# Kernel optimization log

Measured on AMD Instinct MI355X. Metric: run time of the kernel, lower is better.

The kernel has to match this reference:

```python
import jax, jax.numpy as jnp
import numpy as np

SEQ, HID, IN, THETA = 4096, 512, 512, 5


def setup_inputs() -> dict:
    key = jax.random.key(0)
    k0, k1, k2, k3, k4 = jax.random.split(key, 5)
    return {
        "input": jax.random.normal(k0, (1, SEQ, IN), jnp.float32),
        "internal": jax.random.normal(k1, (THETA + 1, SEQ, HID), jnp.float32) * 0.1,
        "state": jnp.zeros((1, 1, HID), jnp.float32),
        "W_ih": jax.random.normal(k2, (HID, IN), jnp.float32) / np.sqrt(IN).astype(np.float32),
        "W_hh": jax.random.normal(k3, (HID, HID), jnp.float32) / np.sqrt(HID).astype(np.float32),
        "b": jax.random.normal(k4, (HID,), jnp.float32) * 0.01,
        "theta": THETA,
    }


def reference(input, internal, state, W_ih, W_hh, b, theta):
    # Unbatched path (batched=False), continuousTheta=False, trunc >= seq (no detach).
    # Cell: h' = tanh(x @ W_ih.T + h @ W_hh.T + b + noise); out = h'.
    x = input[0]                      # [S, I]
    pre_x = x @ W_ih.T + b            # [S, H] precompute input drive
    h0 = state[0, 0]                  # [H]

    # Main recurrence over the sequence (theta index 0 of internal drives it).
    def step(h, px_n):
        px, n = px_n
        h_new = jnp.tanh(px + h @ W_hh.T + n)
        return h_new, h_new

    _, hs = jax.lax.scan(step, h0, (pre_x, internal[0]))   # hs: [S, H]

    # Theta rollouts: padded input is zero, so drive = b + noise. The rollout at
    # every timestep starts from that timestep's main state -> vectorize over S
    # and scan over the theta axis.
    def roll(H, n):
        H_new = jnp.tanh(b + H @ W_hh.T + n)
        return H_new, H_new

    _, Hs = jax.lax.scan(roll, hs, internal[1:])           # Hs: [theta, S, H]

    outputs = jnp.concatenate([hs[None], Hs], axis=0)      # [theta+1, S, H]
    final_state = hs[-1][None, None]                        # [1, 1, H]
    return outputs, final_state
```

## Files before the change

kernel.cpp:

```cpp
#include <hip/hip_runtime.h>
#include <cstdint>
#include <cstddef>

#define SEQ 4096
#define HID 512
#define NTHETA 5
#define NBLK 4
#define RPB 128
#define SENT_BITS 0x40000000u

typedef unsigned long long u64;

__device__ __forceinline__ float tanh_fast(float x) {
  x = fminf(fmaxf(x, -20.0f), 20.0f);
  const float e = __expf(2.0f * x);
  return (e - 1.0f) / (e + 1.0f);
}

__device__ __forceinline__ uint4 load_x4_sc1(const unsigned* p) {
  uint4 u;
  asm volatile("global_load_dwordx4 %0, %1, off sc1\n\ts_waitcnt vmcnt(0)"
               : "=v"(u) : "v"(p) : "memory");
  return u;
}

__device__ __forceinline__ float red16(float v) {
  int p;
  p = __builtin_amdgcn_update_dpp(0, __float_as_int(v), 0xB1, 0xF, 0xF, true);
  v += __int_as_float(p);
  p = __builtin_amdgcn_update_dpp(0, __float_as_int(v), 0x4E, 0xF, 0xF, true);
  v += __int_as_float(p);
  v += __int_as_float(__builtin_amdgcn_ds_swizzle(__float_as_int(v), 0x101F));
  p = __builtin_amdgcn_update_dpp(0, __float_as_int(v), 0x128, 0xF, 0xF, true);
  v += __int_as_float(p);
  return v;
}

__device__ __forceinline__ int swz(int f) {
  return (f & ~7) | ((f ^ (f >> 3)) & 7);
}

__global__ __launch_bounds__(256) void gemm_bias_noise(
    const float* __restrict__ A, const float* __restrict__ W,
    const float* __restrict__ bias, const float* __restrict__ noise,
    float* __restrict__ C, int K, int doTanh)
{
  const int N = HID;
  const int bm = blockIdx.y, bn = blockIdx.x;
  const int tid = threadIdx.x;
  const int tx = tid & 15, ty = tid >> 4;
  const int row0 = bm * 64, col0 = bn * 64;
  __shared__ float As[16][68];
  __shared__ float Ws[16][68];
  float acc[4][4] = {{0.f, 0.f, 0.f, 0.f}, {0.f, 0.f, 0.f, 0.f},
                     {0.f, 0.f, 0.f, 0.f}, {0.f, 0.f, 0.f, 0.f}};
  const int lrow = tid >> 2, lkq = tid & 3;
  for (int kt = 0; kt < K; kt += 16) {
    const float4 av = *(const float4*)&A[(size_t)(row0 + lrow) * K + kt + lkq * 4];
    const float4 wv = *(const float4*)&W[(size_t)(col0 + lrow) * K + kt + lkq * 4];
    __syncthreads();
    As[lkq * 4 + 0][lrow] = av.x; As[lkq * 4 + 1][lrow] = av.y;
    As[lkq * 4 + 2][lrow] = av.z; As[lkq * 4 + 3][lrow] = av.w;
    Ws[lkq * 4 + 0][lrow] = wv.x; Ws[lkq * 4 + 1][lrow] = wv.y;
    Ws[lkq * 4 + 2][lrow] = wv.z; Ws[lkq * 4 + 3][lrow] = wv.w;
    __syncthreads();
#pragma unroll
    for (int k = 0; k < 16; ++k) {
      const float4 a = *(const float4*)&As[k][ty * 4];
      const float4 bq = *(const float4*)&Ws[k][tx * 4];
      const float a4[4] = {a.x, a.y, a.z, a.w};
      const float b4[4] = {bq.x, bq.y, bq.z, bq.w};
#pragma unroll
      for (int i = 0; i < 4; ++i)
#pragma unroll
        for (int j = 0; j < 4; ++j)
          acc[i][j] = fmaf(a4[i], b4[j], acc[i][j]);
    }
  }
  const float4 bv = *(const float4*)&bias[col0 + tx * 4];
#pragma unroll
  for (int i = 0; i < 4; ++i) {
    const int row = row0 + ty * 4 + i;
    const float4 nv = *(const float4*)&noise[(size_t)row * N + col0 + tx * 4];
    float4 o;
    o.x = acc[i][0] + bv.x + nv.x;
    o.y = acc[i][1] + bv.y + nv.y;
    o.z = acc[i][2] + bv.z + nv.z;
    o.w = acc[i][3] + bv.w + nv.w;
    if (doTanh) {
      o.x = tanh_fast(o.x); o.y = tanh_fast(o.y);
      o.z = tanh_fast(o.z); o.w = tanh_fast(o.w);
    }
    *(float4*)&C[(size_t)row * N + col0 + tx * 4] = o;
  }
}

__global__ void fill_sentinel(uint4* __restrict__ p, int n4) {
  const int i = blockIdx.x * blockDim.x + threadIdx.x;
  if (i < n4) p[i] = make_uint4(SENT_BITS, SENT_BITS, SENT_BITS, SENT_BITS);
}

__global__ __launch_bounds__(1024, 4) void recurrence(
    const float* __restrict__ Whh, const float* __restrict__ drive,
    const float* __restrict__ h0, unsigned* __restrict__ hexch)
{
  const int blk = blockIdx.x;
  const int base = blk * RPB;
  const int tid = threadIdx.x;
  const int i = tid >> 4;
  const int j = tid & 15;
  const int r0 = base + 2 * i;

  __shared__ __align__(16) float hbuf[2][HID];

  float4 w0[8], w1[8];
#pragma unroll
  for (int c = 0; c < 8; ++c) {
    w0[c] = *(const float4*)&Whh[(size_t)r0 * HID + 32 * j + 4 * c];
    w1[c] = *(const float4*)&Whh[(size_t)(r0 + 1) * HID + 32 * j + 4 * c];
  }

  const int ch = (tid < blk * 32) ? tid : tid + 32;
  const int wslot = swz(ch);
  const int z0 = swz(r0 >> 2) * 4 + (r0 & 3);

  if (tid < HID) hbuf[0][swz(tid >> 2) * 4 + (tid & 3)] = h0[tid];

  for (int t = 0; t < SEQ; ++t) {
    const int buf = t & 1;

    float2 dr = make_float2(0.f, 0.f);
    if (j == 0) dr = *(const float2*)&drive[(size_t)t * HID + r0];

    if (t > 0 && tid < 96) {
      const unsigned* src = &hexch[(size_t)(t - 1) * HID + 4 * ch];
      uint4 u = load_x4_sc1(src);
      int it = 0;
      while (u.x == SENT_BITS || u.y == SENT_BITS ||
             u.z == SENT_BITS || u.w == SENT_BITS) {
        if ((++it & 7) == 0) {
          u.x = __hip_atomic_load(src + 0, __ATOMIC_RELAXED,
                                  __HIP_MEMORY_SCOPE_AGENT);
          u.y = __hip_atomic_load(src + 1, __ATOMIC_RELAXED,
                                  __HIP_MEMORY_SCOPE_AGENT);
          u.z = __hip_atomic_load(src + 2, __ATOMIC_RELAXED,
                                  __HIP_MEMORY_SCOPE_AGENT);
          u.w = __hip_atomic_load(src + 3, __ATOMIC_RELAXED,
                                  __HIP_MEMORY_SCOPE_AGENT);
        } else {
          u = load_x4_sc1(src);
        }
      }
      ((uint4*)hbuf[buf])[wslot] = u;
    }
    __syncthreads();
    asm volatile("" :: "v"(dr.x), "v"(dr.y));

    float a00 = 0.f, a01 = 0.f, a02 = 0.f, a03 = 0.f;
    float a10 = 0.f, a11 = 0.f, a12 = 0.f, a13 = 0.f;
#pragma unroll
    for (int c = 0; c < 8; ++c) {
      const float4 h4 = *(const float4*)&hbuf[buf][(8 * j + ((c ^ j) & 7)) * 4];
      a00 = fmaf(w0[c].x, h4.x, a00);
      a01 = fmaf(w0[c].y, h4.y, a01);
      a02 = fmaf(w0[c].z, h4.z, a02);
      a03 = fmaf(w0[c].w, h4.w, a03);
      a10 = fmaf(w1[c].x, h4.x, a10);
      a11 = fmaf(w1[c].y, h4.y, a11);
      a12 = fmaf(w1[c].z, h4.z, a12);
      a13 = fmaf(w1[c].w, h4.w, a13);
    }
    float s0 = red16((a00 + a01) + (a02 + a03));
    float s1 = red16((a10 + a11) + (a12 + a13));

    if (j == 0) {
      const float y0 = tanh_fast(s0 + dr.x);
      const float y1 = tanh_fast(s1 + dr.y);
      const u64 pk = (u64)__float_as_uint(y0) | ((u64)__float_as_uint(y1) << 32);
      __hip_atomic_store((u64*)&hexch[(size_t)t * HID + r0], pk,
                         __ATOMIC_RELAXED, __HIP_MEMORY_SCOPE_AGENT);
      *(float2*)&hbuf[buf ^ 1][z0] = make_float2(y0, y1);
    }
  }
}

__global__ void copy_final(const float* __restrict__ src, float* __restrict__ dst) {
  dst[threadIdx.x] = src[threadIdx.x];
}

extern "C" void kernel_launch(void* const* d_in, const int* in_sizes, int n_in,
                              void* d_out, int out_size, void* d_ws, size_t ws_size,
                              hipStream_t stream) {
  const float* input    = (const float*)d_in[0];
  const float* internal = (const float*)d_in[1];
  const float* state    = (const float*)d_in[2];
  const float* W_ih     = (const float*)d_in[3];
  const float* W_hh     = (const float*)d_in[4];
  const float* bias     = (const float*)d_in[5];
  float* out = (float*)d_out;

  const size_t plane = (size_t)SEQ * HID;
  unsigned* hexch = (unsigned*)out;
  float*    drive = out + 5 * plane;

  fill_sentinel<<<(SEQ * HID / 4 + 255) / 256, 256, 0, stream>>>(
      (uint4*)hexch, SEQ * HID / 4);

  dim3 gg(HID / 64, SEQ / 64);
  gemm_bias_noise<<<gg, 256, 0, stream>>>(input, W_ih, bias, internal, drive,
                                          HID, 0);
  recurrence<<<NBLK, 1024, 0, stream>>>(W_hh, drive, state, hexch);
  for (int k = 0; k < NTHETA; ++k) {
    gemm_bias_noise<<<gg, 256, 0, stream>>>(out + (size_t)k * plane, W_hh, bias,
                                            internal + (size_t)(k + 1) * plane,
                                            out + (size_t)(k + 1) * plane,
                                            HID, 1);
  }
  copy_final<<<1, HID, 0, stream>>>(out + (size_t)4095 * HID, out + 6 * plane);
}
```

Measured before the change: 6.509 ms.

## Split recurrence across eight blocks with replicated mailbox planes for exchange

The sequential recurrence now runs on 8 blocks of 512 threads, each owning 64 rows instead of 128. Every new hidden-state pair is written to four replicated mailbox planes plus plane 0, and each block polls its own mailbox copy, which is meant to spread polling contention across more memory locations. Poll loops fall back to plane 0 after many iterations. The cost is four extra atomic stores per step, a larger sentinel fill covering five planes, and more blocks that must synchronise every timestep.

```diff
diff --git a/kernel.cpp b/kernel.cpp
--- a/kernel.cpp
+++ b/kernel.cpp
@@ -5,8 +5,9 @@
 #define SEQ 4096
 #define HID 512
 #define NTHETA 5
-#define NBLK 4
-#define RPB 128
+#define NBLK 8
+#define RPB 64
+#define NMAIL 4
 #define SENT_BITS 0x40000000u
 
 typedef unsigned long long u64;
@@ -21,6 +22,30 @@
   uint4 u;
   asm volatile("global_load_dwordx4 %0, %1, off sc1\n\ts_waitcnt vmcnt(0)"
                : "=v"(u) : "v"(p) : "memory");
+  return u;
+}
+
+__device__ __forceinline__ bool has_sent(uint4 u) {
+  return u.x == SENT_BITS || u.y == SENT_BITS ||
+         u.z == SENT_BITS || u.w == SENT_BITS;
+}
+
+__device__ __forceinline__ uint4 poll_chunk(const unsigned* src,
+                                            const unsigned* safe) {
+  uint4 u = load_x4_sc1(src);
+  int it = 0;
+  while (has_sent(u)) {
+    ++it;
+    if ((it & 7) == 0) {
+      const unsigned* s = (it >= 4096) ? safe : src;
+      u.x = __hip_atomic_load(s + 0, __ATOMIC_RELAXED, __HIP_MEMORY_SCOPE_AGENT);
+      u.y = __hip_atomic_load(s + 1, __ATOMIC_RELAXED, __HIP_MEMORY_SCOPE_AGENT);
+      u.z = __hip_atomic_load(s + 2, __ATOMIC_RELAXED, __HIP_MEMORY_SCOPE_AGENT);
+      u.w = __hip_atomic_load(s + 3, __ATOMIC_RELAXED, __HIP_MEMORY_SCOPE_AGENT);
+    } else {
+      u = load_x4_sc1(src);
+    }
+  }
   return u;
 }
 
@@ -100,10 +125,12 @@
   if (i < n4) p[i] = make_uint4(SENT_BITS, SENT_BITS, SENT_BITS, SENT_BITS);
 }
 
-__global__ __launch_bounds__(1024, 4) void recurrence(
+__global__ __launch_bounds__(512, 2) void recurrence(
     const float* __restrict__ Whh, const float* __restrict__ drive,
-    const float* __restrict__ h0, unsigned* __restrict__ hexch)
+    const float* __restrict__ h0, unsigned* __restrict__ plane0,
+    unsigned* __restrict__ mail)
 {
+  const size_t PL = (size_t)SEQ * HID;
   const int blk = blockIdx.x;
   const int base = blk * RPB;
   const int tid = threadIdx.x;
@@ -113,18 +140,20 @@
 
   __shared__ __align__(16) float hbuf[2][HID];
 
-  float4 w0[8], w1[8];
-#pragma unroll
-  for (int c = 0; c < 8; ++c) {
-    w0[c] = *(const float4*)&Whh[(size_t)r0 * HID + 32 * j + 4 * c];
-    w1[c] = *(const float4*)&Whh[(size_t)(r0 + 1) * HID + 32 * j + 4 * c];
-  }
-
-  const int ch = (tid < blk * 32) ? tid : tid + 32;
+  float w0[32], w1[32];
+  {
+    const volatile float* p0 = &Whh[(size_t)r0 * HID + 32 * j];
+    const volatile float* p1 = p0 + HID;
+#pragma unroll
+    for (int c = 0; c < 32; ++c) { w0[c] = p0[c]; w1[c] = p1[c]; }
+  }
+
+  const int ch = (tid < blk * 16) ? tid : tid + 16;
   const int wslot = swz(ch);
   const int z0 = swz(r0 >> 2) * 4 + (r0 & 3);
-
-  if (tid < HID) hbuf[0][swz(tid >> 2) * 4 + (tid & 3)] = h0[tid];
+  unsigned* mymail = mail + (size_t)(blk & 3) * PL;
+
+  hbuf[0][swz(tid >> 2) * 4 + (tid & 3)] = h0[tid];
 
   for (int t = 0; t < SEQ; ++t) {
     const int buf = t & 1;
@@ -132,25 +161,10 @@
     float2 dr = make_float2(0.f, 0.f);
     if (j == 0) dr = *(const float2*)&drive[(size_t)t * HID + r0];
 
-    if (t > 0 && tid < 96) {
-      const unsigned* src = &hexch[(size_t)(t - 1) * HID + 4 * ch];
-      uint4 u = load_x4_sc1(src);
-      int it = 0;
-      while (u.x == SENT_BITS || u.y == SENT_BITS ||
-             u.z == SENT_BITS || u.w == SENT_BITS) {
-        if ((++it & 7) == 0) {
-          u.x = __hip_atomic_load(src + 0, __ATOMIC_RELAXED,
-                                  __HIP_MEMORY_SCOPE_AGENT);
-          u.y = __hip_atomic_load(src + 1, __ATOMIC_RELAXED,
-                                  __HIP_MEMORY_SCOPE_AGENT);
-          u.z = __hip_atomic_load(src + 2, __ATOMIC_RELAXED,
-                                  __HIP_MEMORY_SCOPE_AGENT);
-          u.w = __hip_atomic_load(src + 3, __ATOMIC_RELAXED,
-                                  __HIP_MEMORY_SCOPE_AGENT);
-        } else {
-          u = load_x4_sc1(src);
-        }
-      }
+    if (t > 0 && tid < 112) {
+      const unsigned* src  = &mymail[(size_t)(t - 1) * HID + 4 * ch];
+      const unsigned* safe = &plane0[(size_t)(t - 1) * HID + 4 * ch];
+      const uint4 u = poll_chunk(src, safe);
       ((uint4*)hbuf[buf])[wslot] = u;
     }
     __syncthreads();
@@ -161,14 +175,14 @@
 #pragma unroll
     for (int c = 0; c < 8; ++c) {
       const float4 h4 = *(const float4*)&hbuf[buf][(8 * j + ((c ^ j) & 7)) * 4];
-      a00 = fmaf(w0[c].x, h4.x, a00);
-      a01 = fmaf(w0[c].y, h4.y, a01);
-      a02 = fmaf(w0[c].z, h4.z, a02);
-      a03 = fmaf(w0[c].w, h4.w, a03);
-      a10 = fmaf(w1[c].x, h4.x, a10);
-      a11 = fmaf(w1[c].y, h4.y, a11);
-      a12 = fmaf(w1[c].z, h4.z, a12);
-      a13 = fmaf(w1[c].w, h4.w, a13);
+      a00 = fmaf(w0[4 * c + 0], h4.x, a00);
+      a01 = fmaf(w0[4 * c + 1], h4.y, a01);
+      a02 = fmaf(w0[4 * c + 2], h4.z, a02);
+      a03 = fmaf(w0[4 * c + 3], h4.w, a03);
+      a10 = fmaf(w1[4 * c + 0], h4.x, a10);
+      a11 = fmaf(w1[4 * c + 1], h4.y, a11);
+      a12 = fmaf(w1[4 * c + 2], h4.z, a12);
+      a13 = fmaf(w1[4 * c + 3], h4.w, a13);
     }
     float s0 = red16((a00 + a01) + (a02 + a03));
     float s1 = red16((a10 + a11) + (a12 + a13));
@@ -177,7 +191,12 @@
       const float y0 = tanh_fast(s0 + dr.x);
       const float y1 = tanh_fast(s1 + dr.y);
       const u64 pk = (u64)__float_as_uint(y0) | ((u64)__float_as_uint(y1) << 32);
-      __hip_atomic_store((u64*)&hexch[(size_t)t * HID + r0], pk,
+      const size_t off = (size_t)t * HID + r0;
+#pragma unroll
+      for (int m = 0; m < NMAIL; ++m)
+        __hip_atomic_store((u64*)&mail[m * PL + off], pk,
+                           __ATOMIC_RELAXED, __HIP_MEMORY_SCOPE_AGENT);
+      __hip_atomic_store((u64*)&plane0[off], pk,
                          __ATOMIC_RELAXED, __HIP_MEMORY_SCOPE_AGENT);
       *(float2*)&hbuf[buf ^ 1][z0] = make_float2(y0, y1);
     }
@@ -200,16 +219,17 @@
   float* out = (float*)d_out;
 
   const size_t plane = (size_t)SEQ * HID;
-  unsigned* hexch = (unsigned*)out;
-  float*    drive = out + 5 * plane;
-
-  fill_sentinel<<<(SEQ * HID / 4 + 255) / 256, 256, 0, stream>>>(
-      (uint4*)hexch, SEQ * HID / 4);
+  unsigned* plane0 = (unsigned*)out;
+  unsigned* mail   = (unsigned*)(out + plane);
+  float*    drive  = out + 5 * plane;
+
+  fill_sentinel<<<((int)(5 * plane / 4) + 255) / 256, 256, 0, stream>>>(
+      (uint4*)out, (int)(5 * plane / 4));
 
   dim3 gg(HID / 64, SEQ / 64);
   gemm_bias_noise<<<gg, 256, 0, stream>>>(input, W_ih, bias, internal, drive,
                                           HID, 0);
-  recurrence<<<NBLK, 1024, 0, stream>>>(W_hh, drive, state, hexch);
+  recurrence<<<NBLK, 512, 0, stream>>>(W_hh, drive, state, plane0, mail);
   for (int k = 0; k < NTHETA; ++k) {
     gemm_bias_noise<<<gg, 256, 0, stream>>>(out + (size_t)k * plane, W_hh, bias,
                                             internal + (size_t)(k + 1) * plane,
```

After: 6.197 ms. 1.05x faster.
